# Performance work log

Hardware: AMD Instinct MI355X
Metric: run time of the kernel (lower is better)

The kernel has to match this reference:

```python
import jax, jax.numpy as jnp
import numpy as np


def setup_inputs() -> dict:
    key = jax.random.key(0)
    generated_images = jax.random.normal(key, (64, 3, 256, 256), dtype=jnp.float32)
    return {"generated_images": generated_images}


def reference(generated_images):
    # Original: sum_{i<j} mse(x_i, x_j), mse = mean over per-image elements.
    # Vectorized via Gram matrix: mean((xi-xj)^2) = (|xi|^2 + |xj|^2 - 2 xi.xj)/D
    B = generated_images.shape[0]
    x = generated_images.reshape(B, -1)          # [B, D]
    D = x.shape[1]
    sq = jnp.sum(x * x, axis=-1)                 # [B]
    G = x @ x.T                                  # [B, B]
    pair = sq[:, None] + sq[None, :] - 2.0 * G   # [B, B], squared L2 distances
    # sum over i<j = (sum of all entries - trace)/2; trace is exactly 0
    sum_pairs = jnp.sum(pair) * 0.5 / D
    return -sum_pairs / (B * (B - 1))
```

## Files before the change

kernel.cpp:

```cpp
#include <hip/hip_runtime.h>
#include <hip/hip_bf16.h>


#define NBLK 768

__global__ __launch_bounds__(256) void div_main(const float4* __restrict__ x4,
                                                float* __restrict__ partial,
                                                int D4) {
    const int lane = threadIdx.x & 63;
    const int rg   = threadIdx.x >> 6;
    const int col  = blockIdx.x * 64 + lane;

    const float4* p = x4 + (size_t)rg * 16 * (size_t)D4 + col;

    float sx = 0.f, sy = 0.f, sz = 0.f, sw = 0.f;
    float sq = 0.f;

    #pragma unroll
    for (int r = 0; r < 16; ++r) {
        float4 v = p[(size_t)r * (size_t)D4];
        sx += v.x; sy += v.y; sz += v.z; sw += v.w;
        sq = fmaf(v.x, v.x, sq);
        sq = fmaf(v.y, v.y, sq);
        sq = fmaf(v.z, v.z, sq);
        sq = fmaf(v.w, v.w, sq);
    }

    float contrib = -64.0f * sq;

    __shared__ float4 part[3][64];
    if (rg > 0) part[rg - 1][lane] = make_float4(sx, sy, sz, sw);
    __syncthreads();
    if (rg == 0) {
        #pragma unroll
        for (int g = 0; g < 3; ++g) {
            float4 t = part[g][lane];
            sx += t.x; sy += t.y; sz += t.z; sw += t.w;
        }
        contrib += sx * sx + sy * sy + sz * sz + sw * sw;
    }

    #pragma unroll
    for (int off = 32; off > 0; off >>= 1)
        contrib += __shfl_down(contrib, off, 64);

    __shared__ float wsum[4];
    if (lane == 0) wsum[rg] = contrib;
    __syncthreads();
    if (threadIdx.x == 0)
        partial[blockIdx.x] = wsum[0] + wsum[1] + wsum[2] + wsum[3];
}

__global__ __launch_bounds__(256) void div_finalize(const float* __restrict__ partial,
                                                    float* __restrict__ out,
                                                    float scale) {
    const int t = threadIdx.x;
    float v = partial[t] + partial[t + 256] + partial[t + 512];

    #pragma unroll
    for (int off = 32; off > 0; off >>= 1)
        v += __shfl_down(v, off, 64);

    __shared__ float wsum[4];
    if ((t & 63) == 0) wsum[t >> 6] = v;
    __syncthreads();
    if (t == 0)
        out[0] = (wsum[0] + wsum[1] + wsum[2] + wsum[3]) * scale;
}

extern "C" void kernel_launch(void* const* d_in, const int* in_sizes, int n_in,
                              void* d_out, int out_size, void* d_ws, size_t ws_size,
                              hipStream_t stream) {
    const float* x = (const float*)d_in[0];
    float* out = (float*)d_out;
    float* partial = (float*)d_ws;

    const int B = 64;
    const int total = in_sizes[0];
    const int D = total / B;
    const int D4 = D / 4;

    const float scale = (float)(1.0 / ((double)D * (double)B * (double)(B - 1)));

    div_main<<<NBLK, 256, 0, stream>>>((const float4*)x, partial, D4);
    div_finalize<<<1, 256, 0, stream>>>(partial, out, scale);
}
```

Baseline: 79.33 us.

## Have each thread reduce all 64 rows of a column, dropping shared-memory merge

Reorganises the work split so each thread walks all 64 images for one float4 column. This removes the cross-wave shared-memory reduction of per-column sums. Grid shrinks to 256 blocks of 192 threads, and the finalize kernel reads one partial per thread. Fewer resident waves per CU may reduce memory-level parallelism in exchange for less synchronisation.

```diff
diff --git a/kernel.cpp b/kernel.cpp
--- a/kernel.cpp
+++ b/kernel.cpp
@@ -1,61 +1,48 @@
 #include <hip/hip_runtime.h>
-#include <hip/hip_bf16.h>
 
 
-#define NBLK 768
+#define NBLK 256
+#define NTHR 192
 
-__global__ __launch_bounds__(256) void div_main(const float4* __restrict__ x4,
-                                                float* __restrict__ partial,
-                                                int D4) {
-    const int lane = threadIdx.x & 63;
-    const int rg   = threadIdx.x >> 6;
-    const int col  = blockIdx.x * 64 + lane;
+__global__ __launch_bounds__(NTHR) void div_main(const float4* __restrict__ x4,
+                                                 float* __restrict__ partial,
+                                                 int D4) {
+    const int col = blockIdx.x * NTHR + threadIdx.x;
+    const float4* p = x4 + col;
 
-    const float4* p = x4 + (size_t)rg * 16 * (size_t)D4 + col;
-
-    float sx = 0.f, sy = 0.f, sz = 0.f, sw = 0.f;
+    float4 acc = make_float4(0.f, 0.f, 0.f, 0.f);
     float sq = 0.f;
 
-    #pragma unroll
-    for (int r = 0; r < 16; ++r) {
+    #pragma unroll 16
+    for (int r = 0; r < 64; ++r) {
         float4 v = p[(size_t)r * (size_t)D4];
-        sx += v.x; sy += v.y; sz += v.z; sw += v.w;
+        acc.x += v.x; acc.y += v.y; acc.z += v.z; acc.w += v.w;
         sq = fmaf(v.x, v.x, sq);
         sq = fmaf(v.y, v.y, sq);
         sq = fmaf(v.z, v.z, sq);
         sq = fmaf(v.w, v.w, sq);
     }
 
-    float contrib = -64.0f * sq;
-
-    __shared__ float4 part[3][64];
-    if (rg > 0) part[rg - 1][lane] = make_float4(sx, sy, sz, sw);
-    __syncthreads();
-    if (rg == 0) {
-        #pragma unroll
-        for (int g = 0; g < 3; ++g) {
-            float4 t = part[g][lane];
-            sx += t.x; sy += t.y; sz += t.z; sw += t.w;
-        }
-        contrib += sx * sx + sy * sy + sz * sz + sw * sw;
-    }
+    float contrib = acc.x * acc.x + acc.y * acc.y + acc.z * acc.z + acc.w * acc.w
+                  - 64.0f * sq;
 
     #pragma unroll
     for (int off = 32; off > 0; off >>= 1)
         contrib += __shfl_down(contrib, off, 64);
 
-    __shared__ float wsum[4];
-    if (lane == 0) wsum[rg] = contrib;
+    __shared__ float wsum[3];
+    const int wave = threadIdx.x >> 6;
+    if ((threadIdx.x & 63) == 0) wsum[wave] = contrib;
     __syncthreads();
     if (threadIdx.x == 0)
-        partial[blockIdx.x] = wsum[0] + wsum[1] + wsum[2] + wsum[3];
+        partial[blockIdx.x] = wsum[0] + wsum[1] + wsum[2];
 }
 
 __global__ __launch_bounds__(256) void div_finalize(const float* __restrict__ partial,
                                                     float* __restrict__ out,
                                                     float scale) {
     const int t = threadIdx.x;
-    float v = partial[t] + partial[t + 256] + partial[t + 512];
+    float v = partial[t];
 
     #pragma unroll
     for (int off = 32; off > 0; off >>= 1)
@@ -82,6 +69,6 @@
 
     const float scale = (float)(1.0 / ((double)D * (double)B * (double)(B - 1)));
 
-    div_main<<<NBLK, 256, 0, stream>>>((const float4*)x, partial, D4);
+    div_main<<<NBLK, NTHR, 0, stream>>>((const float4*)x, partial, D4);
     div_finalize<<<1, 256, 0, stream>>>(partial, out, scale);
 }
```

After: 80.01 us, median of 2. About the same (+0.9%).
